# Kernel optimization log

Measured on AMD Instinct MI355X. Metric: run time of the kernel, lower is better.

The kernel has to match this reference:

```python
import jax, jax.numpy as jnp
import numpy as np

B, N, DIM, H = 4, 8192, 1024, 16
HD = DIM // H
DFF = 4 * DIM
EPS_LN = 1e-5
EPS_NORM = 1e-6


def _layernorm(x, w, b):
    mu = jnp.mean(x, axis=-1, keepdims=True)
    var = jnp.mean(jnp.square(x - mu), axis=-1, keepdims=True)
    return (x - mu) * jax.lax.rsqrt(var + EPS_LN) * w + b


def _phi(x):
    # elu feature map: elu(x) + 1
    return jax.nn.elu(x) + 1.0


def setup_inputs() -> dict:
    key = jax.random.key(0)
    ks = jax.random.split(key, 8)
    s = 0.02
    return {
        "src": jax.random.normal(ks[0], (B, N, DIM), jnp.float32),
        "ln1_w": jnp.ones((DIM,), jnp.float32),
        "ln1_b": jnp.zeros((DIM,), jnp.float32),
        "wq": jax.random.normal(ks[1], (DIM, DIM), jnp.float32) * s,
        "wk": jax.random.normal(ks[2], (DIM, DIM), jnp.float32) * s,
        "wv": jax.random.normal(ks[3], (DIM, DIM), jnp.float32) * s,
        "wo": jax.random.normal(ks[4], (DIM, DIM), jnp.float32) * s,
        "ln2_w": jnp.ones((DIM,), jnp.float32),
        "ln2_b": jnp.zeros((DIM,), jnp.float32),
        "fc1_w": jax.random.normal(ks[5], (DIM, DFF), jnp.float32) * s,
        "fc1_b": jnp.zeros((DFF,), jnp.float32),
        "fc2_w": jax.random.normal(ks[6], (DFF, DIM), jnp.float32) * s,
        "fc2_b": jnp.zeros((DIM,), jnp.float32),
    }


def _linear_attention(x, wq, wk, wv, wo):
    # x: [B, N, DIM]; self-attention (query=key=value=x)
    q = (x @ wq).reshape(B, N, H, HD).transpose(0, 2, 1, 3)  # bhnd
    k = (x @ wk).reshape(B, N, H, HD).transpose(0, 2, 1, 3)
    v = (x @ wv).reshape(B, N, H, HD).transpose(0, 2, 1, 3)
    q = _phi(q)
    k = _phi(k)
    kv = jnp.einsum('bhsd,bhse->bhde', k, v)        # [B,H,HD,HD]
    out = jnp.einsum('bhqd,bhde->bhqe', q, kv)      # [B,H,N,HD]
    k_sum = jnp.sum(k, axis=2)                      # [B,H,HD]
    normalizer = jnp.einsum('bhqd,bhd->bhq', q, k_sum)[..., None] + EPS_NORM
    out = out / normalizer
    out = out.transpose(0, 2, 1, 3).reshape(B, N, DIM)
    return out @ wo


def reference(src, ln1_w, ln1_b, wq, wk, wv, wo, ln2_w, ln2_b, fc1_w, fc1_b, fc2_w, fc2_b):
    # forward_pre: pre-norm transformer block with linear (elu) attention
    h = _layernorm(src, ln1_w, ln1_b)
    src = src + _linear_attention(h, wq, wk, wv, wo)
    h = _layernorm(src, ln2_w, ln2_b)
    h = jax.nn.gelu(h @ fc1_w + fc1_b, approximate=False)  # torch nn.GELU exact
    src = src + (h @ fc2_w + fc2_b)
    return src
```

## Files before the change

### kernel.cpp

```cpp
#include <hip/hip_runtime.h>
#include <hip/hip_bf16.h>

typedef __attribute__((ext_vector_type(8))) short s16x8;
typedef __attribute__((ext_vector_type(4))) short s16x4;
typedef __attribute__((ext_vector_type(8))) __bf16 bf16x8;
typedef __attribute__((ext_vector_type(4))) float f32x4;

__device__ __forceinline__ float b2f(short s) {
  union { float f; unsigned u; } x;
  x.u = ((unsigned)(unsigned short)s) << 16;
  return x.f;
}
__device__ __forceinline__ short f2b(float f) {
  union { float f; unsigned u; } x;
  x.f = f;
  unsigned r = x.u + 0x7fff + ((x.u >> 16) & 1);
  return (short)(r >> 16);
}
__device__ __forceinline__ bf16x8 asbf(s16x8 v) {
  union { s16x8 s; bf16x8 b; } u; u.s = v; return u.b;
}

#define GLD16(g, l) __builtin_amdgcn_global_load_lds( \
    (const __attribute__((address_space(1))) void*)(g), \
    (__attribute__((address_space(3))) void*)(l), 16, 0, 0)

#define WAITB(N) do { \
  asm volatile("s_waitcnt vmcnt(" #N ")" ::: "memory"); \
  __builtin_amdgcn_s_barrier(); \
  asm volatile("" ::: "memory"); \
} while (0)

__global__ __launch_bounds__(256) void transpose_cvt(
    const float* __restrict__ in, short* __restrict__ out, int R, int C) {
  __shared__ float tile[32][33];
  const int tx = threadIdx.x & 31, ty = threadIdx.x >> 5;
  const int c0 = blockIdx.x * 32, r0 = blockIdx.y * 32;
  #pragma unroll
  for (int i = 0; i < 32; i += 8)
    tile[ty + i][tx] = in[(size_t)(r0 + ty + i) * C + c0 + tx];
  __syncthreads();
  #pragma unroll
  for (int i = 0; i < 32; i += 8)
    out[(size_t)(c0 + ty + i) * R + r0 + tx] = f2b(tile[tx][ty + i]);
}

__global__ __launch_bounds__(256) void ln_kernel(
    const float* __restrict__ x, const float* __restrict__ gw,
    const float* __restrict__ gb, short* __restrict__ out) {
  const int row = blockIdx.x;
  const int tid = threadIdx.x;
  const float4 v = ((const float4*)(x + (size_t)row * 1024))[tid];
  float s = v.x + v.y + v.z + v.w;
  float s2 = v.x * v.x + v.y * v.y + v.z * v.z + v.w * v.w;
  #pragma unroll
  for (int o = 32; o > 0; o >>= 1) {
    s += __shfl_xor(s, o);
    s2 += __shfl_xor(s2, o);
  }
  __shared__ float red[2][4];
  const int lane = tid & 63, wid = tid >> 6;
  if (lane == 0) { red[0][wid] = s; red[1][wid] = s2; }
  __syncthreads();
  s = red[0][0] + red[0][1] + red[0][2] + red[0][3];
  s2 = red[1][0] + red[1][1] + red[1][2] + red[1][3];
  const float mu = s * (1.f / 1024.f);
  const float rstd = rsqrtf(s2 * (1.f / 1024.f) - mu * mu + 1e-5f);
  const float4 wv4 = ((const float4*)gw)[tid];
  const float4 bv4 = ((const float4*)gb)[tid];
  s16x4 o4;
  o4.x = f2b((v.x - mu) * rstd * wv4.x + bv4.x);
  o4.y = f2b((v.y - mu) * rstd * wv4.y + bv4.y);
  o4.z = f2b((v.z - mu) * rstd * wv4.z + bv4.z);
  o4.w = f2b((v.w - mu) * rstd * wv4.w + bv4.w);
  *(s16x4*)(out + (size_t)row * 1024 + tid * 4) = o4;
}

__global__ __launch_bounds__(256) void ln_kernel_b(
    const short* __restrict__ x, const float* __restrict__ gw,
    const float* __restrict__ gb, short* __restrict__ out) {
  const int row = blockIdx.x;
  const int tid = threadIdx.x;
  const s16x4 xv = *(const s16x4*)(x + (size_t)row * 1024 + tid * 4);
  float v0 = b2f(xv.x), v1 = b2f(xv.y), v2 = b2f(xv.z), v3 = b2f(xv.w);
  float s = v0 + v1 + v2 + v3;
  float s2 = v0 * v0 + v1 * v1 + v2 * v2 + v3 * v3;
  #pragma unroll
  for (int o = 32; o > 0; o >>= 1) {
    s += __shfl_xor(s, o);
    s2 += __shfl_xor(s2, o);
  }
  __shared__ float red[2][4];
  const int lane = tid & 63, wid = tid >> 6;
  if (lane == 0) { red[0][wid] = s; red[1][wid] = s2; }
  __syncthreads();
  s = red[0][0] + red[0][1] + red[0][2] + red[0][3];
  s2 = red[1][0] + red[1][1] + red[1][2] + red[1][3];
  const float mu = s * (1.f / 1024.f);
  const float rstd = rsqrtf(s2 * (1.f / 1024.f) - mu * mu + 1e-5f);
  const float4 wv4 = ((const float4*)gw)[tid];
  const float4 bv4 = ((const float4*)gb)[tid];
  s16x4 o4;
  o4.x = f2b((v0 - mu) * rstd * wv4.x + bv4.x);
  o4.y = f2b((v1 - mu) * rstd * wv4.y + bv4.y);
  o4.z = f2b((v2 - mu) * rstd * wv4.z + bv4.z);
  o4.w = f2b((v3 - mu) * rstd * wv4.w + bv4.w);
  *(s16x4*)(out + (size_t)row * 1024 + tid * 4) = o4;
}


enum { EPI_QKV = 0, EPI_RES = 1, EPI_GELU = 2, EPI_FC2 = 3 };

#define PHASE(BUFB, MH, KS, LOADB) do { \
    const int ab = (BUFB) + (KS) * 16384; \
    const int bb = (BUFB) + 32768 + (KS) * 16384; \
    if (LOADB) { \
      _Pragma("unroll") \
      for (int n = 0; n < 4; n++) { \
        const int row = wnCol + n * 16 + fr; \
        const int g = row >> 1; \
        const int s = (((row & 1) << 2) | fq) ^ (g & 7); \
        bfv[n] = *(const bf16x8*)(ldsc + bb + g * 128 + s * 16); \
      } \
    } \
    bf16x8 af[4]; \
    _Pragma("unroll") \
    for (int mm = 0; mm < 4; mm++) { \
      const int row = wmRow + (MH) * 64 + mm * 16 + fr; \
      const int g = row >> 1; \
      const int s = (((row & 1) << 2) | fq) ^ (g & 7); \
      af[mm] = *(const bf16x8*)(ldsc + ab + g * 128 + s * 16); \
    } \
    __builtin_amdgcn_s_setprio(1); \
    _Pragma("unroll") \
    for (int mm = 0; mm < 4; mm++) \
      _Pragma("unroll") \
      for (int n = 0; n < 4; n++) \
        acc[(MH) * 4 + mm][n] = __builtin_amdgcn_mfma_f32_16x16x32_bf16( \
            af[mm], bfv[n], acc[(MH) * 4 + mm][n], 0, 0, 0); \
    __builtin_amdgcn_s_setprio(0); \
  } while (0)

template <int EPI>
__global__ __launch_bounds__(512, 2) void gemm256(
    const short* __restrict__ A, int lda,
    const short* __restrict__ Bt, int K, int ldo, int gx,
    const float* __restrict__ bias,
    const void* __restrict__ resid,
    void* __restrict__ outp) {
  __shared__ alignas(16) short lds[65536];
  const int tid = threadIdx.x;
  const int lane = tid & 63, wave = tid >> 6;
  const int cpx = (int)gridDim.x >> 3;
  const int bid = ((int)blockIdx.x & 7) * cpx + ((int)blockIdx.x >> 3);
  const int sgx = gx >> 3;
  const int grp = bid >> 5;
  const int sm = grp % sgx, sn = grp / sgx;
  const int bm = (sm * 8 + (bid & 7)) * 256;
  const int bn = (sn * 4 + ((bid & 31) >> 3)) * 256;
  const int wmRow = (wave >> 2) * 128;
  const int wnCol = (wave & 3) * 64;
  const int fr = lane & 15, fq = lane >> 4;

  const int sg = tid >> 3;
  const int s0 = (tid & 7) ^ (sg & 7);
  const int srow = 2 * sg + (s0 >> 2);
  const int scol = (s0 & 3) * 8;
  const int sdst = tid * 16;

  const char* ldsc = (const char*)lds;
  char* ldsw = (char*)lds;

  f32x4 acc[8][4] = {};
  bf16x8 bfv[4];

  auto stageA = [&](int bufb, int kh, int kk) {
    const short* g = A + (size_t)(bm + srow) * lda + kk + kh * 32 + scol;
    char* l = ldsw + bufb + kh * 16384 + sdst;
    GLD16(g, l);
    GLD16(g + (size_t)128 * lda, l + 8192);
  };
  auto stageB = [&](int bufb, int kh, int kk) {
    const short* g = Bt + (size_t)(bn + srow) * K + kk + kh * 32 + scol;
    char* l = ldsw + bufb + 32768 + kh * 16384 + sdst;
    GLD16(g, l);
    GLD16(g + (size_t)128 * K, l + 8192);
  };

  const int NT = K >> 6;
  stageA(0, 0, 0);
  stageB(0, 0, 0);
  stageA(0, 1, 0);
  stageB(0, 1, 0);
  WAITB(4);

  int buf = 0;
  for (int t = 0; t < NT; ++t) {
    const int kkn = (t + 1 < NT) ? ((t + 1) << 6) : 0;
    const int nb = buf ^ 65536;
    stageA(nb, 0, kkn);
    PHASE(buf, 0, 0, true);
    stageB(nb, 0, kkn);
    PHASE(buf, 1, 0, false);
    WAITB(8);
    stageA(nb, 1, kkn);
    PHASE(buf, 0, 1, true);
    stageB(nb, 1, kkn);
    PHASE(buf, 1, 1, false);
    WAITB(4);
    buf = nb;
  }
  asm volatile("s_waitcnt vmcnt(0)" ::: "memory");

  const int row0 = bm + wmRow + fq * 4;
  const int col0 = bn + wnCol + fr;
  #pragma unroll
  for (int m = 0; m < 8; m++) {
    #pragma unroll
    for (int n = 0; n < 4; n++) {
      const int col = col0 + n * 16;
      #pragma unroll
      for (int r = 0; r < 4; r++) {
        const int row = row0 + m * 16 + r;
        float v = acc[m][n][r];
        if constexpr (EPI == EPI_QKV) {
          if (col < 2048) v = (v > 0.f) ? (v + 1.f) : __expf(v);
          ((short*)outp)[(size_t)row * ldo + col] = f2b(v);
        } else if constexpr (EPI == EPI_RES) {
          ((short*)outp)[(size_t)row * ldo + col] =
              f2b(v + ((const float*)resid)[(size_t)row * ldo + col]);
        } else if constexpr (EPI == EPI_GELU) {
          v += bias[col];
          v = 0.5f * v * (1.f + erff(v * 0.70710678118654752f));
          ((short*)outp)[(size_t)row * ldo + col] = f2b(v);
        } else {
          v += bias[col] + b2f(((const short*)resid)[(size_t)row * ldo + col]);
          ((float*)outp)[(size_t)row * ldo + col] = v;
        }
      }
    }
  }
}

__global__ __launch_bounds__(256) void kv_reduce(
    const short* __restrict__ qkv, float* __restrict__ kv_part,
    float* __restrict__ ksum_part) {
  const int blk = blockIdx.x;
  const int bh = blk >> 6, chunk = blk & 63;
  const int b = bh >> 4, h = bh & 15;
  const size_t rowbase = (size_t)b * 8192 + (size_t)chunk * 128;
  const int kcol = 1024 + h * 64, vcol = 2048 + h * 64;
  __shared__ float Klf[64][68];
  __shared__ float Vlf[64][68];
  const int tid = threadIdx.x;
  const int dk = tid >> 2, dq = tid & 3;
  float acc[16] = {};
  float ks = 0.f;
  for (int t = 0; t < 2; t++) {
    #pragma unroll
    for (int i = 0; i < 2; i++) {
      const int s = i * 256 + tid;
      const int r = s >> 3, seg = (s & 7) * 8;
      const size_t g = (rowbase + t * 64 + r) * 3072;
      const s16x8 k8 = *(const s16x8*)&qkv[g + kcol + seg];
      const s16x8 v8 = *(const s16x8*)&qkv[g + vcol + seg];
      float4 ka, kb, va, vb;
      ka.x = b2f(k8[0]); ka.y = b2f(k8[1]); ka.z = b2f(k8[2]); ka.w = b2f(k8[3]);
      kb.x = b2f(k8[4]); kb.y = b2f(k8[5]); kb.z = b2f(k8[6]); kb.w = b2f(k8[7]);
      va.x = b2f(v8[0]); va.y = b2f(v8[1]); va.z = b2f(v8[2]); va.w = b2f(v8[3]);
      vb.x = b2f(v8[4]); vb.y = b2f(v8[5]); vb.z = b2f(v8[6]); vb.w = b2f(v8[7]);
      *(float4*)&Klf[r][seg] = ka;
      *(float4*)&Klf[r][seg + 4] = kb;
      *(float4*)&Vlf[r][seg] = va;
      *(float4*)&Vlf[r][seg + 4] = vb;
    }
    __syncthreads();
    #pragma unroll 4
    for (int n = 0; n < 64; n++) {
      const float kval = Klf[n][dk];
      if (dq == 0) ks += kval;
      const float4 v0 = *(const float4*)&Vlf[n][dq * 16];
      const float4 v1 = *(const float4*)&Vlf[n][dq * 16 + 4];
      const float4 v2 = *(const float4*)&Vlf[n][dq * 16 + 8];
      const float4 v3 = *(const float4*)&Vlf[n][dq * 16 + 12];
      acc[0]  = fmaf(kval, v0.x, acc[0]);
      acc[1]  = fmaf(kval, v0.y, acc[1]);
      acc[2]  = fmaf(kval, v0.z, acc[2]);
      acc[3]  = fmaf(kval, v0.w, acc[3]);
      acc[4]  = fmaf(kval, v1.x, acc[4]);
      acc[5]  = fmaf(kval, v1.y, acc[5]);
      acc[6]  = fmaf(kval, v1.z, acc[6]);
      acc[7]  = fmaf(kval, v1.w, acc[7]);
      acc[8]  = fmaf(kval, v2.x, acc[8]);
      acc[9]  = fmaf(kval, v2.y, acc[9]);
      acc[10] = fmaf(kval, v2.z, acc[10]);
      acc[11] = fmaf(kval, v2.w, acc[11]);
      acc[12] = fmaf(kval, v3.x, acc[12]);
      acc[13] = fmaf(kval, v3.y, acc[13]);
      acc[14] = fmaf(kval, v3.z, acc[14]);
      acc[15] = fmaf(kval, v3.w, acc[15]);
    }
    __syncthreads();
  }
  float* dst = kv_part + (size_t)blk * 4096 + dk * 64 + dq * 16;
  #pragma unroll
  for (int j = 0; j < 16; j++) dst[j] = acc[j];
  if (dq == 0) ksum_part[(size_t)blk * 64 + dk] = ks;
}

__global__ __launch_bounds__(256) void kv_finalize(
    const float* __restrict__ kv_part, const float* __restrict__ ksum_part,
    short* __restrict__ kvT_g, float* __restrict__ ksum_f) {
  const int bh = blockIdx.x >> 2, dg = blockIdx.x & 3;
  const int tid = threadIdx.x;
  const int e = tid & 63, j4 = tid >> 6;
  const int d0 = dg * 16 + j4 * 4;
  float a0 = 0.f, a1 = 0.f, a2 = 0.f, a3 = 0.f;
  const float* base = kv_part + (size_t)bh * 64 * 4096 + d0 * 64 + e;
  for (int c = 0; c < 64; c++) {
    const float* p = base + (size_t)c * 4096;
    a0 += p[0]; a1 += p[64]; a2 += p[128]; a3 += p[192];
  }
  s16x4 o; o.x = f2b(a0); o.y = f2b(a1); o.z = f2b(a2); o.w = f2b(a3);
  char* dstb = (char*)(kvT_g + (size_t)bh * 4096);
  *(s16x4*)(dstb + e * 128 + ((2 * d0) ^ ((e & 7) << 4))) = o;
  if (tid < 16) {
    const int d = dg * 16 + tid;
    float s = 0.f;
    for (int c = 0; c < 64; c++)
      s += ksum_part[((size_t)bh * 64 + c) * 64 + d];
    ksum_f[bh * 64 + d] = s;
  }
}

__global__ __launch_bounds__(256) void attn_apply_mfma(
    const short* __restrict__ qkv, const short* __restrict__ kvT_g,
    const float* __restrict__ ksum_f, short* __restrict__ ao) {
  __shared__ alignas(16) short kvs[4096];
  __shared__ float ksl[64];
  const int blk = blockIdx.x;
  const int bh = blk >> 5, rc = blk & 31;
  const int b = bh >> 4, h = bh & 15;
  const int tid = threadIdx.x, lane = tid & 63, w = tid >> 6;
  const int fr = lane & 15, fq = lane >> 4;

  GLD16(kvT_g + (size_t)bh * 4096 + tid * 8, (char*)kvs + tid * 16);
  GLD16(kvT_g + (size_t)bh * 4096 + (256 + tid) * 8, (char*)kvs + (256 + tid) * 16);
  if (tid < 64) ksl[tid] = ksum_f[bh * 64 + tid];
  __syncthreads();

  bf16x8 bkv[4][2], bns[2];
  #pragma unroll
  for (int n = 0; n < 4; n++) {
    #pragma unroll
    for (int c = 0; c < 2; c++) {
      const int e = n * 16 + fr;
      const int byteoff = e * 128 + ((c * 64 + fq * 16) ^ ((e & 7) << 4));
      bkv[n][c] = *(const bf16x8*)((const char*)kvs + byteoff);
    }
  }
  #pragma unroll
  for (int c = 0; c < 2; c++) {
    s16x8 ts = {0, 0, 0, 0, 0, 0, 0, 0};
    if (fr == 0) {
      #pragma unroll
      for (int j = 0; j < 8; j++) ts[j] = f2b(ksl[c * 32 + fq * 8 + j]);
    }
    bns[c] = asbf(ts);
  }

  f32x4 acc[4][4] = {};
  f32x4 nacc[4] = {};
  const size_t rowbase = (size_t)b * 8192 + (size_t)rc * 256 + w * 64;
  const int qcol = h * 64;
  #pragma unroll
  for (int m = 0; m < 4; m++) {
    const short* qrow = qkv + (rowbase + m * 16 + fr) * 3072 + qcol + fq * 8;
    const bf16x8 a0 = *(const bf16x8*)qrow;
    const bf16x8 a1 = *(const bf16x8*)(qrow + 32);
    #pragma unroll
    for (int n = 0; n < 4; n++) {
      acc[m][n] = __builtin_amdgcn_mfma_f32_16x16x32_bf16(a0, bkv[n][0], acc[m][n], 0, 0, 0);
      acc[m][n] = __builtin_amdgcn_mfma_f32_16x16x32_bf16(a1, bkv[n][1], acc[m][n], 0, 0, 0);
    }
    nacc[m] = __builtin_amdgcn_mfma_f32_16x16x32_bf16(a0, bns[0], nacc[m], 0, 0, 0);
    nacc[m] = __builtin_amdgcn_mfma_f32_16x16x32_bf16(a1, bns[1], nacc[m], 0, 0, 0);
  }

  #pragma unroll
  for (int m = 0; m < 4; m++) {
    #pragma unroll
    for (int r = 0; r < 4; r++) {
      const float nv = __shfl(nacc[m][r], lane & 48) + 1e-6f;
      const float rn = 1.f / nv;
      const size_t row = rowbase + m * 16 + fq * 4 + r;
      #pragma unroll
      for (int n = 0; n < 4; n++)
        ao[row * 1024 + qcol + n * 16 + fr] = f2b(acc[m][n][r] * rn);
    }
  }
}

extern "C" void kernel_launch(void* const* d_in, const int* in_sizes, int n_in,
                              void* d_out, int out_size, void* d_ws, size_t ws_size,
                              hipStream_t stream) {
  (void)in_sizes; (void)n_in; (void)out_size; (void)ws_size;
  const float* src   = (const float*)d_in[0];
  const float* ln1_w = (const float*)d_in[1];
  const float* ln1_b = (const float*)d_in[2];
  const float* wq    = (const float*)d_in[3];
  const float* wk    = (const float*)d_in[4];
  const float* wv    = (const float*)d_in[5];
  const float* wo    = (const float*)d_in[6];
  const float* ln2_w = (const float*)d_in[7];
  const float* ln2_b = (const float*)d_in[8];
  const float* fc1_w = (const float*)d_in[9];
  const float* fc1_b = (const float*)d_in[10];
  const float* fc2_w = (const float*)d_in[11];
  const float* fc2_b = (const float*)d_in[12];

  char* ws = (char*)d_ws;
  short* wqkvT     = (short*)(ws + 0);
  short* woT       = (short*)(ws + 6291456);
  short* fc1T      = (short*)(ws + 8388608);
  short* fc2T      = (short*)(ws + 16777216);
  short* kvT_g     = (short*)(ws + 25165824);
  float* ksum_f    = (float*)(ws + 25690112);
  float* kv_part   = (float*)(ws + 25706496);
  float* ksum_part = (float*)(ws + 92815360);
  short* hbuf      = (short*)(ws + 93863936);
  short* src2b     = (short*)(ws + 160972800);
  short* qkv       = (short*)(ws + 295190528);
  short* a1c       = (short*)(ws + 295190528);

  const dim3 tb(256);
  const dim3 tb512(512);

  transpose_cvt<<<dim3(32, 32), tb, 0, stream>>>(wq, wqkvT, 1024, 1024);
  transpose_cvt<<<dim3(32, 32), tb, 0, stream>>>(wk, wqkvT + 1024 * 1024, 1024, 1024);
  transpose_cvt<<<dim3(32, 32), tb, 0, stream>>>(wv, wqkvT + 2048 * 1024, 1024, 1024);
  transpose_cvt<<<dim3(32, 32), tb, 0, stream>>>(wo, woT, 1024, 1024);
  transpose_cvt<<<dim3(128, 32), tb, 0, stream>>>(fc1_w, fc1T, 1024, 4096);
  transpose_cvt<<<dim3(32, 128), tb, 0, stream>>>(fc2_w, fc2T, 4096, 1024);

  ln_kernel<<<32768, tb, 0, stream>>>(src, ln1_w, ln1_b, hbuf);

  gemm256<EPI_QKV><<<dim3(1536), tb512, 0, stream>>>(
      hbuf, 1024, wqkvT, 1024, 3072, 128, nullptr, nullptr, qkv);

  kv_reduce<<<4096, tb, 0, stream>>>(qkv, kv_part, ksum_part);
  kv_finalize<<<256, tb, 0, stream>>>(kv_part, ksum_part, kvT_g, ksum_f);

  attn_apply_mfma<<<2048, tb, 0, stream>>>(qkv, kvT_g, ksum_f, hbuf);

  gemm256<EPI_RES><<<dim3(512), tb512, 0, stream>>>(
      hbuf, 1024, woT, 1024, 1024, 128, nullptr, src, src2b);

  ln_kernel_b<<<32768, tb, 0, stream>>>(src2b, ln2_w, ln2_b, hbuf);

  for (int c = 0; c < 2; c++) {
    const size_t mo = (size_t)c * 16384;
    gemm256<EPI_GELU><<<dim3(1024), tb512, 0, stream>>>(
        hbuf + mo * 1024, 1024, fc1T, 1024, 4096, 64, fc1_b, nullptr, a1c);
    gemm256<EPI_FC2><<<dim3(256), tb512, 0, stream>>>(
        a1c, 4096, fc2T, 4096, 1024, 64, fc2_b, src2b + mo * 1024,
        (float*)d_out + mo * 1024);
  }
}
```

Before: 1.128 ms.

## Switch GEMM to 32x32x16 MFMA and coarsen kv_reduce chunks

The GEMM inner phase now uses 32x32x16 bf16 MFMA instructions with 32x32 fragments instead of 16x16x32. This cuts the LDS fragment loads per MFMA and the instruction count, and the accumulator layout and epilogue indexing are remapped to match. Separately, kv_reduce now gives each block a 512-row chunk instead of 128, so there are four times fewer partials for kv_finalize to write and sum. The larger chunks also mean fewer blocks, which lowers parallelism in kv_reduce.

```diff
diff --git a/kernel.cpp b/kernel.cpp
--- a/kernel.cpp
+++ b/kernel.cpp
@@ -5,6 +5,7 @@
 typedef __attribute__((ext_vector_type(4))) short s16x4;
 typedef __attribute__((ext_vector_type(8))) __bf16 bf16x8;
 typedef __attribute__((ext_vector_type(4))) float f32x4;
+typedef __attribute__((ext_vector_type(16))) float f32x16;
 
 __device__ __forceinline__ float b2f(short s) {
   union { float f; unsigned u; } x;
@@ -116,28 +117,36 @@
     const int bb = (BUFB) + 32768 + (KS) * 16384; \
     if (LOADB) { \
       _Pragma("unroll") \
-      for (int n = 0; n < 4; n++) { \
-        const int row = wnCol + n * 16 + fr; \
+      for (int cf = 0; cf < 2; cf++) \
+        _Pragma("unroll") \
+        for (int w = 0; w < 2; w++) { \
+          const int row = wnCol + cf * 32 + l31; \
+          const int g = row >> 1; \
+          const int q = 2 * w + lh; \
+          const int s = (((row & 1) << 2) | q) ^ (g & 7); \
+          bfvw[cf][w] = *(const bf16x8*)(ldsc + bb + g * 128 + s * 16); \
+        } \
+    } \
+    bf16x8 af[2][2]; \
+    _Pragma("unroll") \
+    for (int rf = 0; rf < 2; rf++) \
+      _Pragma("unroll") \
+      for (int w = 0; w < 2; w++) { \
+        const int row = wmRow + ((MH) * 2 + rf) * 32 + l31; \
         const int g = row >> 1; \
-        const int s = (((row & 1) << 2) | fq) ^ (g & 7); \
-        bfv[n] = *(const bf16x8*)(ldsc + bb + g * 128 + s * 16); \
+        const int q = 2 * w + lh; \
+        const int s = (((row & 1) << 2) | q) ^ (g & 7); \
+        af[rf][w] = *(const bf16x8*)(ldsc + ab + g * 128 + s * 16); \
       } \
-    } \
-    bf16x8 af[4]; \
-    _Pragma("unroll") \
-    for (int mm = 0; mm < 4; mm++) { \
-      const int row = wmRow + (MH) * 64 + mm * 16 + fr; \
-      const int g = row >> 1; \
-      const int s = (((row & 1) << 2) | fq) ^ (g & 7); \
-      af[mm] = *(const bf16x8*)(ldsc + ab + g * 128 + s * 16); \
-    } \
     __builtin_amdgcn_s_setprio(1); \
     _Pragma("unroll") \
-    for (int mm = 0; mm < 4; mm++) \
+    for (int w = 0; w < 2; w++) \
       _Pragma("unroll") \
-      for (int n = 0; n < 4; n++) \
-        acc[(MH) * 4 + mm][n] = __builtin_amdgcn_mfma_f32_16x16x32_bf16( \
-            af[mm], bfv[n], acc[(MH) * 4 + mm][n], 0, 0, 0); \
+      for (int rf = 0; rf < 2; rf++) \
+        _Pragma("unroll") \
+        for (int cf = 0; cf < 2; cf++) \
+          acc[(MH) * 2 + rf][cf] = __builtin_amdgcn_mfma_f32_32x32x16_bf16( \
+              af[rf][w], bfvw[cf][w], acc[(MH) * 2 + rf][cf], 0, 0, 0); \
     __builtin_amdgcn_s_setprio(0); \
   } while (0)
 
@@ -160,7 +169,7 @@
   const int bn = (sn * 4 + ((bid & 31) >> 3)) * 256;
   const int wmRow = (wave >> 2) * 128;
   const int wnCol = (wave & 3) * 64;
-  const int fr = lane & 15, fq = lane >> 4;
+  const int l31 = lane & 31, lh = lane >> 5;
 
   const int sg = tid >> 3;
   const int s0 = (tid & 7) ^ (sg & 7);
@@ -171,8 +180,8 @@
   const char* ldsc = (const char*)lds;
   char* ldsw = (char*)lds;
 
-  f32x4 acc[8][4] = {};
-  bf16x8 bfv[4];
+  f32x16 acc[4][2] = {};
+  bf16x8 bfvw[2][2];
 
   auto stageA = [&](int bufb, int kh, int kk) {
     const short* g = A + (size_t)(bm + srow) * lda + kk + kh * 32 + scol;
@@ -212,17 +221,17 @@
   }
   asm volatile("s_waitcnt vmcnt(0)" ::: "memory");
 
-  const int row0 = bm + wmRow + fq * 4;
-  const int col0 = bn + wnCol + fr;
-  #pragma unroll
-  for (int m = 0; m < 8; m++) {
+  const int colbase = bn + wnCol + l31;
+  const int rowbase0 = bm + wmRow + 4 * lh;
+  #pragma unroll
+  for (int rf = 0; rf < 4; rf++) {
     #pragma unroll
-    for (int n = 0; n < 4; n++) {
-      const int col = col0 + n * 16;
+    for (int cf = 0; cf < 2; cf++) {
+      const int col = colbase + cf * 32;
       #pragma unroll
-      for (int r = 0; r < 4; r++) {
-        const int row = row0 + m * 16 + r;
-        float v = acc[m][n][r];
+      for (int reg = 0; reg < 16; reg++) {
+        const int row = rowbase0 + rf * 32 + (reg & 3) + 8 * (reg >> 2);
+        float v = acc[rf][cf][reg];
         if constexpr (EPI == EPI_QKV) {
           if (col < 2048) v = (v > 0.f) ? (v + 1.f) : __expf(v);
           ((short*)outp)[(size_t)row * ldo + col] = f2b(v);
@@ -246,9 +255,9 @@
     const short* __restrict__ qkv, float* __restrict__ kv_part,
     float* __restrict__ ksum_part) {
   const int blk = blockIdx.x;
-  const int bh = blk >> 6, chunk = blk & 63;
+  const int bh = blk >> 4, chunk = blk & 15;
   const int b = bh >> 4, h = bh & 15;
-  const size_t rowbase = (size_t)b * 8192 + (size_t)chunk * 128;
+  const size_t rowbase = (size_t)b * 8192 + (size_t)chunk * 512;
   const int kcol = 1024 + h * 64, vcol = 2048 + h * 64;
   __shared__ float Klf[64][68];
   __shared__ float Vlf[64][68];
@@ -256,7 +265,7 @@
   const int dk = tid >> 2, dq = tid & 3;
   float acc[16] = {};
   float ks = 0.f;
-  for (int t = 0; t < 2; t++) {
+  for (int t = 0; t < 8; t++) {
     #pragma unroll
     for (int i = 0; i < 2; i++) {
       const int s = i * 256 + tid;
@@ -316,8 +325,8 @@
   const int e = tid & 63, j4 = tid >> 6;
   const int d0 = dg * 16 + j4 * 4;
   float a0 = 0.f, a1 = 0.f, a2 = 0.f, a3 = 0.f;
-  const float* base = kv_part + (size_t)bh * 64 * 4096 + d0 * 64 + e;
-  for (int c = 0; c < 64; c++) {
+  const float* base = kv_part + (size_t)bh * 16 * 4096 + d0 * 64 + e;
+  for (int c = 0; c < 16; c++) {
     const float* p = base + (size_t)c * 4096;
     a0 += p[0]; a1 += p[64]; a2 += p[128]; a3 += p[192];
   }
@@ -327,8 +336,8 @@
   if (tid < 16) {
     const int d = dg * 16 + tid;
     float s = 0.f;
-    for (int c = 0; c < 64; c++)
-      s += ksum_part[((size_t)bh * 64 + c) * 64 + d];
+    for (int c = 0; c < 16; c++)
+      s += ksum_part[((size_t)bh * 16 + c) * 64 + d];
     ksum_f[bh * 64 + d] = s;
   }
 }
@@ -427,7 +436,7 @@
   short* kvT_g     = (short*)(ws + 25165824);
   float* ksum_f    = (float*)(ws + 25690112);
   float* kv_part   = (float*)(ws + 25706496);
-  float* ksum_part = (float*)(ws + 92815360);
+  float* ksum_part = (float*)(ws + 42483712);
   short* hbuf      = (short*)(ws + 93863936);
   short* src2b     = (short*)(ws + 160972800);
   short* qkv       = (short*)(ws + 295190528);
@@ -448,7 +457,7 @@
   gemm256<EPI_QKV><<<dim3(1536), tb512, 0, stream>>>(
       hbuf, 1024, wqkvT, 1024, 3072, 128, nullptr, nullptr, qkv);
 
-  kv_reduce<<<4096, tb, 0, stream>>>(qkv, kv_part, ksum_part);
+  kv_reduce<<<1024, tb, 0, stream>>>(qkv, kv_part, ksum_part);
   kv_finalize<<<256, tb, 0, stream>>>(kv_part, ksum_part, kvT_g, ksum_f);
 
   attn_apply_mfma<<<2048, tb, 0, stream>>>(qkv, kvT_g, ksum_f, hbuf);
```

Result: slower. 1.185 ms (+5.0%).
